# Optimization experiments

Hardware: AMD Instinct MI355X
Metric: run time of the kernel (lower is better)

The kernel has to match this reference:

```python
import jax, jax.numpy as jnp
import numpy as np

B, Md, L, SHOTS, UP = 8, 256, 31, 2, 2  # batch, downsampled spatial, bands, shots, upsample factor


def setup_inputs() -> dict:
    key = jax.random.key(0)
    k1, k2 = jax.random.split(key)
    Y = jax.random.uniform(k1, (B, Md, Md + L - 1, SHOTS), dtype=jnp.float32)
    H = jax.random.uniform(k2, (B, Md, Md, L, SHOTS), dtype=jnp.float32)
    return {"Y": Y, "H": H}


def reference(Y, H):
    # CASSI adjoint: X[b,m,n,l,s] = Y[b,m,(n+l) mod N2,s]  (tf.roll(-l) + slice [0:Md])
    N2 = Y.shape[2]  # Md + L - 1
    idx = (jnp.arange(Md)[:, None] + jnp.arange(L)[None, :]) % N2  # (Md, L)
    X = Y[:, :, idx, :]                      # (B, Md, Md, L, SHOTS) gather
    X = jnp.sum(H * X, axis=4)               # mask multiply + sum over shots -> (B, Md, Md, L)
    X = X / jnp.max(X)                        # global-max normalization
    # UpSampling2D(size=(2,2)), nearest, channels_last
    X = jnp.repeat(jnp.repeat(X, UP, axis=1), UP, axis=2)  # (B, 2*Md, 2*Md, L)
    return X
```

## Files before the change

kernel.cpp:

```cpp
#include <hip/hip_runtime.h>

#define NX    16252928u
#define NPAIR 8126464u
#define NOUT  65011712u
#define NOUT4 16252928u

template <bool STORE>
__global__ __launch_bounds__(256) void k_compute_x_max(
    const float4* __restrict__ H4, const float2* __restrict__ Y2,
    float2* __restrict__ X2, int* __restrict__ maxslot)
{
    float m = 0.0f;
    const unsigned stride = gridDim.x * blockDim.x;
    for (unsigned p = blockIdx.x * blockDim.x + threadIdx.x; p < NPAIR; p += stride) {
        unsigned e0 = 2u * p;
        unsigned e1 = e0 + 1u;
        unsigned q0 = e0 / 31u, l0 = e0 - q0 * 31u;
        unsigned q1 = e1 / 31u, l1 = e1 - q1 * 31u;
        unsigned y0 = (q0 >> 8) * 286u + (q0 & 255u) + l0;
        unsigned y1 = (q1 >> 8) * 286u + (q1 & 255u) + l1;
        float4 h  = H4[p];
        float2 ya = Y2[y0];
        float2 yb = Y2[y1];
        float x0 = h.x * ya.x + h.y * ya.y;
        float x1 = h.z * yb.x + h.w * yb.y;
        if (STORE) X2[p] = make_float2(x0, x1);
        m = fmaxf(m, fmaxf(x0, x1));
    }
    #pragma unroll
    for (int off = 32; off > 0; off >>= 1)
        m = fmaxf(m, __shfl_xor(m, off, 64));
    __shared__ float wmax[4];
    const int lane = threadIdx.x & 63, wid = threadIdx.x >> 6;
    if (lane == 0) wmax[wid] = m;
    __syncthreads();
    if (threadIdx.x == 0) {
        float bm = fmaxf(fmaxf(wmax[0], wmax[1]), fmaxf(wmax[2], wmax[3]));
        atomicMax(maxslot, __float_as_int(bm));
    }
}

__global__ __launch_bounds__(256) void k_upsample(
    const float* __restrict__ X, const int* __restrict__ maxslot,
    float4* __restrict__ out)
{
    const float inv = 1.0f / __int_as_float(*maxslot);
    const unsigned stride = gridDim.x * blockDim.x;
    for (unsigned g = blockIdx.x * blockDim.x + threadIdx.x; g < NOUT4; g += stride) {
        const unsigned t = 4u * g;
        float4 v;
        float* vp = &v.x;
        #pragma unroll
        for (int j = 0; j < 4; ++j) {
            unsigned e = t + (unsigned)j;
            unsigned r = e / 31u, l = e - r * 31u;
            unsigned q  = r & 511u;
            unsigned pp = (r >> 9) & 511u;
            unsigned b  = r >> 18;
            unsigned xi = ((((b << 8) + (pp >> 1)) << 8) | (q >> 1)) * 31u + l;
            vp[j] = X[xi] * inv;
        }
        out[g] = v;
    }
}

__global__ __launch_bounds__(256) void k_upsample_recompute(
    const float2* __restrict__ H2, const float2* __restrict__ Y2,
    const int* __restrict__ maxslot, float4* __restrict__ out)
{
    const float inv = 1.0f / __int_as_float(*maxslot);
    const unsigned stride = gridDim.x * blockDim.x;
    for (unsigned g = blockIdx.x * blockDim.x + threadIdx.x; g < NOUT4; g += stride) {
        const unsigned t = 4u * g;
        float4 v;
        float* vp = &v.x;
        #pragma unroll
        for (int j = 0; j < 4; ++j) {
            unsigned e = t + (unsigned)j;
            unsigned r = e / 31u, l = e - r * 31u;
            unsigned q  = r & 511u;
            unsigned pp = (r >> 9) & 511u;
            unsigned b  = r >> 18;
            unsigned m  = pp >> 1, i = q >> 1;
            unsigned bm = (b << 8) + m;
            unsigned hidx = ((bm << 8) + i) * 31u + l;
            unsigned yidx = bm * 286u + i + l;
            float2 h = H2[hidx];
            float2 y = Y2[yidx];
            vp[j] = (h.x * y.x + h.y * y.y) * inv;
        }
        out[g] = v;
    }
}

extern "C" void kernel_launch(void* const* d_in, const int* in_sizes, int n_in,
                              void* d_out, int out_size, void* d_ws, size_t ws_size,
                              hipStream_t stream) {
    const float* Y = (const float*)d_in[0];
    const float* H = (const float*)d_in[1];

    int*    maxslot = (int*)d_ws;
    float2* X2      = (float2*)((char*)d_ws + 256);
    const size_t need = 256 + (size_t)NX * 4;

    const float4* H4 = (const float4*)H;
    const float2* Y2 = (const float2*)Y;
    float4* out4 = (float4*)d_out;

    if (ws_size >= need) {
        k_compute_x_max<true><<<1024, 256, 0, stream>>>(H4, Y2, X2, maxslot);
        k_upsample<<<4096, 256, 0, stream>>>((const float*)X2, maxslot, out4);
    } else {
        k_compute_x_max<false><<<1024, 256, 0, stream>>>(H4, Y2, nullptr, maxslot);
        k_upsample_recompute<<<4096, 256, 0, stream>>>((const float2*)H, Y2, maxslot, out4);
    }
}
```

Measured before the change: 403.9 us.

## Recompute X per tile in shared memory and write each row twice for upsampling

The intermediate X buffer is dropped. The first kernel now only computes the global max. The output kernel gives each block one (b,m) row slice of 32 columns. It recomputes X from H and Y into shared memory, then writes each upsampled float4 to the two duplicated output rows. This removes the X round trip to global memory (a write plus a scattered re-read) and the per-element index math. In exchange H is read twice, once for the max and once for the output. The max kernel grid also grows from 1024 to 2048 blocks.

```diff
diff --git a/kernel.cpp b/kernel.cpp
--- a/kernel.cpp
+++ b/kernel.cpp
@@ -1,31 +1,22 @@
 #include <hip/hip_runtime.h>
 
-#define NX    16252928u
 #define NPAIR 8126464u
-#define NOUT  65011712u
-#define NOUT4 16252928u
 
-template <bool STORE>
-__global__ __launch_bounds__(256) void k_compute_x_max(
+__global__ __launch_bounds__(256) void k_max(
     const float4* __restrict__ H4, const float2* __restrict__ Y2,
-    float2* __restrict__ X2, int* __restrict__ maxslot)
+    int* __restrict__ maxslot)
 {
     float m = 0.0f;
     const unsigned stride = gridDim.x * blockDim.x;
     for (unsigned p = blockIdx.x * blockDim.x + threadIdx.x; p < NPAIR; p += stride) {
-        unsigned e0 = 2u * p;
-        unsigned e1 = e0 + 1u;
+        unsigned e0 = 2u * p, e1 = e0 + 1u;
         unsigned q0 = e0 / 31u, l0 = e0 - q0 * 31u;
         unsigned q1 = e1 / 31u, l1 = e1 - q1 * 31u;
         unsigned y0 = (q0 >> 8) * 286u + (q0 & 255u) + l0;
         unsigned y1 = (q1 >> 8) * 286u + (q1 & 255u) + l1;
-        float4 h  = H4[p];
-        float2 ya = Y2[y0];
-        float2 yb = Y2[y1];
-        float x0 = h.x * ya.x + h.y * ya.y;
-        float x1 = h.z * yb.x + h.w * yb.y;
-        if (STORE) X2[p] = make_float2(x0, x1);
-        m = fmaxf(m, fmaxf(x0, x1));
+        float4 h = H4[p];
+        float2 ya = Y2[y0], yb = Y2[y1];
+        m = fmaxf(m, fmaxf(h.x * ya.x + h.y * ya.y, h.z * yb.x + h.w * yb.y));
     }
     #pragma unroll
     for (int off = 32; off > 0; off >>= 1)
@@ -35,61 +26,48 @@
     if (lane == 0) wmax[wid] = m;
     __syncthreads();
     if (threadIdx.x == 0) {
-        float bm = fmaxf(fmaxf(wmax[0], wmax[1]), fmaxf(wmax[2], wmax[3]));
-        atomicMax(maxslot, __float_as_int(bm));
+        float bmax = fmaxf(fmaxf(wmax[0], wmax[1]), fmaxf(wmax[2], wmax[3]));
+        atomicMax(maxslot, __float_as_int(bmax));
     }
 }
 
-__global__ __launch_bounds__(256) void k_upsample(
-    const float* __restrict__ X, const int* __restrict__ maxslot,
-    float4* __restrict__ out)
+__global__ __launch_bounds__(256) void k_out(
+    const float4* __restrict__ H4, const float2* __restrict__ Y2,
+    const int* __restrict__ maxslot, float4* __restrict__ out4)
 {
+    __shared__ float xs[992];
+    const unsigned bm = blockIdx.x >> 3;
+    const unsigned ti = blockIdx.x & 7u;
     const float inv = 1.0f / __int_as_float(*maxslot);
-    const unsigned stride = gridDim.x * blockDim.x;
-    for (unsigned g = blockIdx.x * blockDim.x + threadIdx.x; g < NOUT4; g += stride) {
-        const unsigned t = 4u * g;
+
+    const unsigned h4base = bm * 3968u + ti * 496u;
+    const unsigned ybase  = bm * 286u + ti * 32u;
+    for (unsigned f2 = threadIdx.x; f2 < 496u; f2 += 256u) {
+        unsigned f  = 2u * f2;
+        unsigned c0 = f / 31u,        l0 = f        - c0 * 31u;
+        unsigned c1 = (f + 1u) / 31u, l1 = (f + 1u) - c1 * 31u;
+        float4 h  = H4[h4base + f2];
+        float2 ya = Y2[ybase + c0 + l0];
+        float2 yb = Y2[ybase + c1 + l1];
+        xs[f]      = h.x * ya.x + h.y * ya.y;
+        xs[f + 1u] = h.z * yb.x + h.w * yb.y;
+    }
+    __syncthreads();
+
+    const unsigned b = bm >> 8, mrow = bm & 255u;
+    float4* r0 = out4 + (size_t)((b * 512u + 2u * mrow) * 3968u + ti * 496u);
+    float4* r1 = r0 + 3968u;
+    for (unsigned g = threadIdx.x; g < 496u; g += 256u) {
         float4 v;
         float* vp = &v.x;
         #pragma unroll
-        for (int j = 0; j < 4; ++j) {
-            unsigned e = t + (unsigned)j;
-            unsigned r = e / 31u, l = e - r * 31u;
-            unsigned q  = r & 511u;
-            unsigned pp = (r >> 9) & 511u;
-            unsigned b  = r >> 18;
-            unsigned xi = ((((b << 8) + (pp >> 1)) << 8) | (q >> 1)) * 31u + l;
-            vp[j] = X[xi] * inv;
+        for (int k = 0; k < 4; ++k) {
+            unsigned s  = 4u * g + (unsigned)k;
+            unsigned oc = s / 31u, r = s - oc * 31u;
+            vp[k] = xs[(oc >> 1) * 31u + r] * inv;
         }
-        out[g] = v;
-    }
-}
-
-__global__ __launch_bounds__(256) void k_upsample_recompute(
-    const float2* __restrict__ H2, const float2* __restrict__ Y2,
-    const int* __restrict__ maxslot, float4* __restrict__ out)
-{
-    const float inv = 1.0f / __int_as_float(*maxslot);
-    const unsigned stride = gridDim.x * blockDim.x;
-    for (unsigned g = blockIdx.x * blockDim.x + threadIdx.x; g < NOUT4; g += stride) {
-        const unsigned t = 4u * g;
-        float4 v;
-        float* vp = &v.x;
-        #pragma unroll
-        for (int j = 0; j < 4; ++j) {
-            unsigned e = t + (unsigned)j;
-            unsigned r = e / 31u, l = e - r * 31u;
-            unsigned q  = r & 511u;
-            unsigned pp = (r >> 9) & 511u;
-            unsigned b  = r >> 18;
-            unsigned m  = pp >> 1, i = q >> 1;
-            unsigned bm = (b << 8) + m;
-            unsigned hidx = ((bm << 8) + i) * 31u + l;
-            unsigned yidx = bm * 286u + i + l;
-            float2 h = H2[hidx];
-            float2 y = Y2[yidx];
-            vp[j] = (h.x * y.x + h.y * y.y) * inv;
-        }
-        out[g] = v;
+        r0[g] = v;
+        r1[g] = v;
     }
 }
 
@@ -99,19 +77,9 @@
     const float* Y = (const float*)d_in[0];
     const float* H = (const float*)d_in[1];
 
-    int*    maxslot = (int*)d_ws;
-    float2* X2      = (float2*)((char*)d_ws + 256);
-    const size_t need = 256 + (size_t)NX * 4;
+    int* maxslot = (int*)d_ws;
 
-    const float4* H4 = (const float4*)H;
-    const float2* Y2 = (const float2*)Y;
-    float4* out4 = (float4*)d_out;
-
-    if (ws_size >= need) {
-        k_compute_x_max<true><<<1024, 256, 0, stream>>>(H4, Y2, X2, maxslot);
-        k_upsample<<<4096, 256, 0, stream>>>((const float*)X2, maxslot, out4);
-    } else {
-        k_compute_x_max<false><<<1024, 256, 0, stream>>>(H4, Y2, nullptr, maxslot);
-        k_upsample_recompute<<<4096, 256, 0, stream>>>((const float2*)H, Y2, maxslot, out4);
-    }
+    k_max<<<2048, 256, 0, stream>>>((const float4*)H, (const float2*)Y, maxslot);
+    k_out<<<8 * 256 * 8, 256, 0, stream>>>((const float4*)H, (const float2*)Y,
+                                           maxslot, (float4*)d_out);
 }
```

Result: faster. 384.8 us (-4.7%).
